# Performance work log

Measured on AMD Instinct MI355X. Metric: run time of the kernel, lower is better.

Reference implementation:

```python
import jax, jax.numpy as jnp
import numpy as np
import math

DIM_K = 64  # head dim used for scaling
NEG = -1000000000.0

def setup_inputs() -> dict:
    key = jax.random.key(0)
    k1, k2, k3, k4 = jax.random.split(key, 4)
    B, H, S, D = 4, 16, 2048, 64
    return {
        "key": jax.random.normal(k1, (B, H, S, D), dtype=jnp.float32),
        "query": jax.random.normal(k2, (B, H, S, D), dtype=jnp.float32),
        "value": jax.random.normal(k3, (B, H, S, D), dtype=jnp.float32),
        "mask": jax.random.randint(k4, (B, S, S), 0, 2, dtype=jnp.int32),
    }

def reference(key, query, value, mask):
    # scores: [B,H,Sq,Sk]
    scores = jnp.einsum('bhqd,bhkd->bhqk', query, key) / math.sqrt(DIM_K)
    scores = jnp.where(mask[:, None, :, :] == 0, NEG, scores)
    attn = jax.nn.softmax(scores, axis=-1)  # dropout is identity in eval mode
    return jnp.einsum('bhqk,bhkd->bhqd', attn, value)
```

## Files before the change

kernel.cpp:

```cpp
#include <hip/hip_runtime.h>
#include <hip/hip_bf16.h>
#include <stdint.h>

#define B_ 4
#define H_ 16
#define S_ 2048
#define D_ 64
#define NKT (S_ / 64)
#define QM 128

typedef __attribute__((ext_vector_type(8))) short bf16x8;
typedef __attribute__((ext_vector_type(4))) float f32x4;
typedef unsigned long long u64;
typedef unsigned int u32;

__device__ inline u32 cvt_pk_bf16(float lo, float hi) {
  u32 r;
  asm("v_cvt_pk_bf16_f32 %0, %1, %2" : "=v"(r) : "v"(lo), "v"(hi));
  return r;
}

__device__ inline int SW(int row, int byteoff) {
  return row * 128 + (byteoff ^ ((row & 7) << 4));
}

__device__ inline void gll16(const void* g, void* l) {
  __builtin_amdgcn_global_load_lds(
      (const __attribute__((address_space(1))) u32*)g,
      (__attribute__((address_space(3))) u32*)(uintptr_t)l, 16, 0, 0);
}

__global__ __launch_bounds__(256)
void prep_k(const float* __restrict__ Kg, char* __restrict__ Ksw) {
  int idx = blockIdx.x * 256 + threadIdx.x;
  int row = idx >> 1, half = idx & 1;
  const float* src = Kg + (size_t)idx * 32;
  float4 v[8];
#pragma unroll
  for (int k = 0; k < 8; ++k) v[k] = *(const float4*)(src + k * 4);
  char* dstrow = Ksw + (size_t)row * 128;
  int xo = (row & 7) << 4;
#pragma unroll
  for (int j = 0; j < 4; ++j) {
    uint4 u;
    u.x = cvt_pk_bf16(v[2 * j].x, v[2 * j].y);
    u.y = cvt_pk_bf16(v[2 * j].z, v[2 * j].w);
    u.z = cvt_pk_bf16(v[2 * j + 1].x, v[2 * j + 1].y);
    u.w = cvt_pk_bf16(v[2 * j + 1].z, v[2 * j + 1].w);
    *(uint4*)(dstrow + (((4 * half + j) * 16) ^ xo)) = u;
  }
}

__global__ __launch_bounds__(256)
void prep_v(const float* __restrict__ Vg, char* __restrict__ Vsw) {
  __shared__ short tile[4096];
  const int vb = blockIdx.x, tid = threadIdx.x;
  char* ct = (char*)tile;
  int c4 = tid & 15, g = tid >> 4;
  const float* src = Vg + (size_t)vb * (64 * D_) + (size_t)(g * 4) * D_ + c4 * 4;
  float4 vv[4];
#pragma unroll
  for (int i = 0; i < 4; ++i) vv[i] = *(const float4*)(src + (size_t)i * D_);
  const float* vf = (const float*)vv;
#pragma unroll
  for (int dd = 0; dd < 4; ++dd) {
    uint2 u;
    u.x = cvt_pk_bf16(vf[0 * 4 + dd], vf[1 * 4 + dd]);
    u.y = cvt_pk_bf16(vf[2 * 4 + dd], vf[3 * 4 + dd]);
    *(uint2*)(ct + SW(c4 * 4 + dd, g * 8)) = u;
  }
  __syncthreads();
  char* dst = Vsw + (size_t)vb * 8192;
#pragma unroll
  for (int j = 0; j < 2; ++j)
    *(float4*)(dst + tid * 16 + j * 4096) = *(const float4*)(ct + tid * 16 + j * 4096);
}

__global__ __launch_bounds__(256)
void prep_m(const int* __restrict__ Mg, u64* __restrict__ Mp) {
  const int tid = threadIdx.x;
  const int lane = tid & 63;
  const int gwave = blockIdx.x * 4 + (tid >> 6);
  for (int c0 = gwave * 4; c0 < (B_ * S_ * S_ / 256); c0 += 4096 * 4) {
    int vals[4][4];
#pragma unroll
    for (int cj = 0; cj < 4; ++cj) {
      const int* src = Mg + (size_t)(c0 + cj) * 256;
#pragma unroll
      for (int j = 0; j < 4; ++j) vals[cj][j] = src[j * 64 + lane];
    }
#pragma unroll
    for (int cj = 0; cj < 4; ++cj) {
      u64 bits[4];
#pragma unroll
      for (int j = 0; j < 4; ++j) bits[j] = __ballot(vals[cj][j] != 0);
      if (lane == 0) {
        ulonglong4 o;
        o.x = bits[0]; o.y = bits[1]; o.z = bits[2]; o.w = bits[3];
        *(ulonglong4*)(Mp + (size_t)(c0 + cj) * 4) = o;
      }
    }
  }
}

__global__ __launch_bounds__(256, 4)
void attn_kernel(const float* __restrict__ Qg,
                 const char* __restrict__ Ksw,
                 const char* __restrict__ Vsw,
                 const u64* __restrict__ Mp,
                 float* __restrict__ Og) {
  __shared__ short sK[2][4096];
  __shared__ short sV[2][4096];

  const int tid  = threadIdx.x;
  const int w    = tid >> 6;
  const int lane = tid & 63;
  const int quad = lane >> 4;
  const int c    = lane & 15;

  const int flat = blockIdx.x + (int)gridDim.x * blockIdx.y;
  const int bh   = (flat & 7) | ((flat >> 7) << 3);
  const int q0   = ((flat >> 3) & 15) * QM;
  const int b    = bh >> 4;

  const size_t base = (size_t)bh * (S_ * D_);
  const char* Kt = Ksw + (size_t)bh * (S_ * 128);
  const char* Vt = Vsw + (size_t)bh * (S_ * 128);
  char* cK0 = (char*)sK;

  const float SC = 0.125f * 1.44269504088896f;
#pragma unroll
  for (int j = 0; j < 8; ++j) {
    int idx = tid + j * 256;
    int row = idx >> 4, c4 = idx & 15;
    float4 v = *(const float4*)(Qg + base + (size_t)(q0 + row) * D_ + c4 * 4);
    uint2 u;
    u.x = cvt_pk_bf16(v.x * SC, v.y * SC);
    u.y = cvt_pk_bf16(v.z * SC, v.w * SC);
    *(uint2*)(cK0 + SW(row, c4 * 8)) = u;
  }
  __syncthreads();
  bf16x8 qa[2][2];
#pragma unroll
  for (int gi = 0; gi < 2; ++gi) {
    qa[gi][0] = *(bf16x8*)(cK0 + SW(32 * w + 16 * gi + c, quad * 16));
    qa[gi][1] = *(bf16x8*)(cK0 + SW(32 * w + 16 * gi + c, 64 + quad * 16));
  }
  __syncthreads();

#pragma unroll
  for (int j = 0; j < 2; ++j) {
    gll16(Kt + tid * 16 + j * 4096, (char*)sK[0] + tid * 16 + j * 4096);
    gll16(Vt + tid * 16 + j * 4096, (char*)sV[0] + tid * 16 + j * 4096);
  }

  int koff[4][2];
#pragma unroll
  for (int n = 0; n < 4; ++n) {
    koff[n][0] = SW(16 * n + c, quad * 16);
    koff[n][1] = SW(16 * n + c, 64 + quad * 16);
  }

  bf16x8 ones;
#pragma unroll
  for (int i = 0; i < 8; ++i) ones[i] = (short)0x3F80;

  f32x4 acco[2][4];
  f32x4 acc_l[2];
#pragma unroll
  for (int gi = 0; gi < 2; ++gi) {
    acc_l[gi] = f32x4{0, 0, 0, 0};
#pragma unroll
    for (int i = 0; i < 4; ++i) acco[gi][i] = f32x4{0, 0, 0, 0};
  }

  const u64* mrowp = Mp + ((size_t)b * S_ + q0 + 32 * w + c) * NKT;

  const char* kbase = (const char*)sK;
  const char* vbase = (const char*)sV;

  for (int kt2 = 0; kt2 < NKT; kt2 += 2) {
#pragma unroll
    for (int p = 0; p < 2; ++p) {
      const int kt = kt2 + p;

      __syncthreads();

      u64 mw[2];
      mw[0] = mrowp[kt];
      mw[1] = mrowp[16 * NKT + kt];

      f32x4 accs[2][4];
      __builtin_amdgcn_s_setprio(1);
#pragma unroll
      for (int n = 0; n < 4; ++n) {
        bf16x8 kb0 = *(bf16x8*)(kbase + koff[n][0] + p * 8192);
        bf16x8 kb1 = *(bf16x8*)(kbase + koff[n][1] + p * 8192);
#pragma unroll
        for (int gi = 0; gi < 2; ++gi) {
          f32x4 z = {0, 0, 0, 0};
          z = __builtin_amdgcn_mfma_f32_16x16x32_bf16(kb0, qa[gi][0], z, 0, 0, 0);
          z = __builtin_amdgcn_mfma_f32_16x16x32_bf16(kb1, qa[gi][1], z, 0, 0, 0);
          accs[gi][n] = z;
        }
      }
      __builtin_amdgcn_s_setprio(0);

      if (kt + 1 < NKT) {
        char* kn = (char*)sK + (p ^ 1) * 8192;
        char* vn = (char*)sV + (p ^ 1) * 8192;
        const char* kg = Kt + (size_t)(kt + 1) * 8192;
        const char* vg = Vt + (size_t)(kt + 1) * 8192;
#pragma unroll
        for (int j = 0; j < 2; ++j) {
          gll16(kg + tid * 16 + j * 4096, kn + tid * 16 + j * 4096);
          gll16(vg + tid * 16 + j * 4096, vn + tid * 16 + j * 4096);
        }
      }

      bf16x8 pa[2][2];
#pragma unroll
      for (int gi = 0; gi < 2; ++gi) {
        u32 mlo = (u32)(mw[gi] >> (4 * quad));
        u32 mhi = (u32)(mw[gi] >> (4 * quad + 32));
        float e[4][4];
#pragma unroll
        for (int n = 0; n < 4; ++n) {
          u32 mword = (n < 2) ? mlo : mhi;
          int sh = 16 * (n & 1);
#pragma unroll
          for (int r = 0; r < 4; ++r) {
            float sm = ((mword >> (sh + r)) & 1u) ? accs[gi][n][r] : -1000.0f;
            e[n][r] = exp2f(sm);
          }
        }

        u32 pk[4][2];
#pragma unroll
        for (int n = 0; n < 4; ++n) {
          pk[n][0] = cvt_pk_bf16(e[n][0], e[n][1]);
          pk[n][1] = cvt_pk_bf16(e[n][2], e[n][3]);
        }

#pragma unroll
        for (int t = 0; t < 2; ++t) {
          union { bf16x8 v; u32 uw[4]; } pu;
#pragma unroll
          for (int h = 0; h < 2; ++h) {
            u32 a  = pk[2 * t][h];
            u32 bq = pk[2 * t + 1][h];
            asm("v_permlane32_swap_b32 %0, %1" : "+v"(a), "+v"(bq));
            asm("v_permlane16_swap_b32 %0, %1" : "+v"(a), "+v"(bq));
            pu.uw[h]     = a;
            pu.uw[2 + h] = bq;
          }
          pa[gi][t] = pu.v;
        }
      }

      __builtin_amdgcn_s_setprio(1);
#pragma unroll
      for (int dn = 0; dn < 4; ++dn) {
        bf16x8 vb0 = *(bf16x8*)(vbase + koff[dn][0] + p * 8192);
        bf16x8 vb1 = *(bf16x8*)(vbase + koff[dn][1] + p * 8192);
#pragma unroll
        for (int gi = 0; gi < 2; ++gi) {
          acco[gi][dn] = __builtin_amdgcn_mfma_f32_16x16x32_bf16(pa[gi][0], vb0, acco[gi][dn], 0, 0, 0);
          acco[gi][dn] = __builtin_amdgcn_mfma_f32_16x16x32_bf16(pa[gi][1], vb1, acco[gi][dn], 0, 0, 0);
        }
      }
#pragma unroll
      for (int gi = 0; gi < 2; ++gi) {
        acc_l[gi] = __builtin_amdgcn_mfma_f32_16x16x32_bf16(pa[gi][0], ones, acc_l[gi], 0, 0, 0);
        acc_l[gi] = __builtin_amdgcn_mfma_f32_16x16x32_bf16(pa[gi][1], ones, acc_l[gi], 0, 0, 0);
      }
      __builtin_amdgcn_s_setprio(0);
    }
  }

#pragma unroll
  for (int gi = 0; gi < 2; ++gi) {
#pragma unroll
    for (int r = 0; r < 4; ++r) {
      float inv = 1.0f / acc_l[gi][r];
      size_t orow = base + (size_t)(q0 + 32 * w + 16 * gi + quad * 4 + r) * D_;
#pragma unroll
      for (int dn = 0; dn < 4; ++dn)
        Og[orow + 16 * dn + c] = acco[gi][dn][r] * inv;
    }
  }
}

extern "C" void kernel_launch(void* const* d_in, const int* in_sizes, int n_in,
                              void* d_out, int out_size, void* d_ws, size_t ws_size,
                              hipStream_t stream) {
  const float* Kg = (const float*)d_in[0];
  const float* Qg = (const float*)d_in[1];
  const float* Vg = (const float*)d_in[2];
  const int*   Mg = (const int*)d_in[3];
  float* Og = (float*)d_out;

  char* ws  = (char*)d_ws;
  u64*  Mp  = (u64*)ws;
  char* Ksw = ws + (size_t)(2u << 20);
  char* Vsw = ws + (size_t)(2u << 20) + (16u << 20);

  prep_k<<<1024, 256, 0, stream>>>(Kg, Ksw);
  prep_v<<<2048, 256, 0, stream>>>(Vg, Vsw);
  prep_m<<<1024, 256, 0, stream>>>(Mg, Mp);
  attn_kernel<<<dim3(S_ / QM, B_ * H_), 256, 0, stream>>>(Qg, Ksw, Vsw, Mp, Og);
}
```

Measured before the change: 305.6 us.

## Split prep and attention into halves and overlap second-half prep with attention

The separate K, V and mask preparation kernels are merged into one device routine that can process either half of the batch-head range. A first kernel preps half 0. A mixed kernel then runs attention on group 0 in 512 blocks while 512 other blocks prep half 1. A final kernel runs attention on group 1. The aim is to hide the memory-bound conversion and mask-packing work behind the compute-bound attention, and to cut the number of launches. The cost is imbalance inside the mixed launch, plus possible contention between attention and prep blocks for memory bandwidth and CU slots.

```diff
diff --git a/kernel.cpp b/kernel.cpp
--- a/kernel.cpp
+++ b/kernel.cpp
@@ -30,96 +30,97 @@
       (__attribute__((address_space(3))) u32*)(uintptr_t)l, 16, 0, 0);
 }
 
-__global__ __launch_bounds__(256)
-void prep_k(const float* __restrict__ Kg, char* __restrict__ Ksw) {
-  int idx = blockIdx.x * 256 + threadIdx.x;
-  int row = idx >> 1, half = idx & 1;
-  const float* src = Kg + (size_t)idx * 32;
-  float4 v[8];
-#pragma unroll
-  for (int k = 0; k < 8; ++k) v[k] = *(const float4*)(src + k * 4);
-  char* dstrow = Ksw + (size_t)row * 128;
-  int xo = (row & 7) << 4;
-#pragma unroll
-  for (int j = 0; j < 4; ++j) {
-    uint4 u;
-    u.x = cvt_pk_bf16(v[2 * j].x, v[2 * j].y);
-    u.y = cvt_pk_bf16(v[2 * j].z, v[2 * j].w);
-    u.z = cvt_pk_bf16(v[2 * j + 1].x, v[2 * j + 1].y);
-    u.w = cvt_pk_bf16(v[2 * j + 1].z, v[2 * j + 1].w);
-    *(uint4*)(dstrow + (((4 * half + j) * 16) ^ xo)) = u;
-  }
-}
-
-__global__ __launch_bounds__(256)
-void prep_v(const float* __restrict__ Vg, char* __restrict__ Vsw) {
-  __shared__ short tile[4096];
-  const int vb = blockIdx.x, tid = threadIdx.x;
-  char* ct = (char*)tile;
-  int c4 = tid & 15, g = tid >> 4;
-  const float* src = Vg + (size_t)vb * (64 * D_) + (size_t)(g * 4) * D_ + c4 * 4;
-  float4 vv[4];
-#pragma unroll
-  for (int i = 0; i < 4; ++i) vv[i] = *(const float4*)(src + (size_t)i * D_);
-  const float* vf = (const float*)vv;
-#pragma unroll
-  for (int dd = 0; dd < 4; ++dd) {
-    uint2 u;
-    u.x = cvt_pk_bf16(vf[0 * 4 + dd], vf[1 * 4 + dd]);
-    u.y = cvt_pk_bf16(vf[2 * 4 + dd], vf[3 * 4 + dd]);
-    *(uint2*)(ct + SW(c4 * 4 + dd, g * 8)) = u;
-  }
-  __syncthreads();
-  char* dst = Vsw + (size_t)vb * 8192;
-#pragma unroll
-  for (int j = 0; j < 2; ++j)
-    *(float4*)(dst + tid * 16 + j * 4096) = *(const float4*)(ct + tid * 16 + j * 4096);
-}
-
-__global__ __launch_bounds__(256)
-void prep_m(const int* __restrict__ Mg, u64* __restrict__ Mp) {
-  const int tid = threadIdx.x;
-  const int lane = tid & 63;
-  const int gwave = blockIdx.x * 4 + (tid >> 6);
-  for (int c0 = gwave * 4; c0 < (B_ * S_ * S_ / 256); c0 += 4096 * 4) {
-    int vals[4][4];
-#pragma unroll
-    for (int cj = 0; cj < 4; ++cj) {
-      const int* src = Mg + (size_t)(c0 + cj) * 256;
-#pragma unroll
-      for (int j = 0; j < 4; ++j) vals[cj][j] = src[j * 64 + lane];
-    }
-#pragma unroll
-    for (int cj = 0; cj < 4; ++cj) {
-      u64 bits[4];
-#pragma unroll
-      for (int j = 0; j < 4; ++j) bits[j] = __ballot(vals[cj][j] != 0);
-      if (lane == 0) {
-        ulonglong4 o;
-        o.x = bits[0]; o.y = bits[1]; o.z = bits[2]; o.w = bits[3];
-        *(ulonglong4*)(Mp + (size_t)(c0 + cj) * 4) = o;
-      }
-    }
-  }
-}
-
-__global__ __launch_bounds__(256, 4)
-void attn_kernel(const float* __restrict__ Qg,
-                 const char* __restrict__ Ksw,
-                 const char* __restrict__ Vsw,
-                 const u64* __restrict__ Mp,
-                 float* __restrict__ Og) {
-  __shared__ short sK[2][4096];
-  __shared__ short sV[2][4096];
-
-  const int tid  = threadIdx.x;
+__device__ inline void dev_prep(int half, int blkL, int tid,
+                                const float* __restrict__ Kg,
+                                const float* __restrict__ Vg,
+                                const int* __restrict__ Mg,
+                                char* __restrict__ Ksw, char* __restrict__ Vsw,
+                                u64* __restrict__ Mp, short* scratch) {
+  {
+    int idxH = half * 131072 + blkL * 256 + tid;
+    int row = idxH >> 1, hh = idxH & 1;
+    const float* src = Kg + (size_t)idxH * 32;
+    float4 v[8];
+#pragma unroll
+    for (int k = 0; k < 8; ++k) v[k] = *(const float4*)(src + k * 4);
+    char* dstrow = Ksw + (size_t)row * 128;
+    int xo = (row & 7) << 4;
+#pragma unroll
+    for (int j = 0; j < 4; ++j) {
+      uint4 u;
+      u.x = cvt_pk_bf16(v[2 * j].x, v[2 * j].y);
+      u.y = cvt_pk_bf16(v[2 * j].z, v[2 * j].w);
+      u.z = cvt_pk_bf16(v[2 * j + 1].x, v[2 * j + 1].y);
+      u.w = cvt_pk_bf16(v[2 * j + 1].z, v[2 * j + 1].w);
+      *(uint4*)(dstrow + (((4 * hh + j) * 16) ^ xo)) = u;
+    }
+  }
+  {
+    char* ct = (char*)scratch;
+    int c4 = tid & 15, g = tid >> 4;
+#pragma unroll
+    for (int it = 0; it < 2; ++it) {
+      int vb = half * 1024 + blkL * 2 + it;
+      const float* src = Vg + (size_t)vb * (64 * D_) + (size_t)(g * 4) * D_ + c4 * 4;
+      float4 vv[4];
+#pragma unroll
+      for (int i = 0; i < 4; ++i) vv[i] = *(const float4*)(src + (size_t)i * D_);
+      const float* vf = (const float*)vv;
+      if (it) __syncthreads();
+#pragma unroll
+      for (int dd = 0; dd < 4; ++dd) {
+        uint2 u;
+        u.x = cvt_pk_bf16(vf[0 * 4 + dd], vf[1 * 4 + dd]);
+        u.y = cvt_pk_bf16(vf[2 * 4 + dd], vf[3 * 4 + dd]);
+        *(uint2*)(ct + SW(c4 * 4 + dd, g * 8)) = u;
+      }
+      __syncthreads();
+      char* dst = Vsw + (size_t)vb * 8192;
+#pragma unroll
+      for (int j = 0; j < 2; ++j)
+        *(float4*)(dst + tid * 16 + j * 4096) = *(const float4*)(ct + tid * 16 + j * 4096);
+    }
+  }
+  {
+    const int lane = tid & 63;
+    const int gw = blkL * 4 + (tid >> 6);
+    const int base = half * 32768;
+    for (int c0 = base + gw * 4; c0 < base + 32768; c0 += 2048 * 4) {
+      int vals[4][4];
+#pragma unroll
+      for (int cj = 0; cj < 4; ++cj) {
+        const int* src = Mg + (size_t)(c0 + cj) * 256;
+#pragma unroll
+        for (int j = 0; j < 4; ++j) vals[cj][j] = src[j * 64 + lane];
+      }
+#pragma unroll
+      for (int cj = 0; cj < 4; ++cj) {
+        u64 bits[4];
+#pragma unroll
+        for (int j = 0; j < 4; ++j) bits[j] = __ballot(vals[cj][j] != 0);
+        if (lane == 0) {
+          ulonglong4 o;
+          o.x = bits[0]; o.y = bits[1]; o.z = bits[2]; o.w = bits[3];
+          *(ulonglong4*)(Mp + (size_t)(c0 + cj) * 4) = o;
+        }
+      }
+    }
+  }
+}
+
+__device__ inline void dev_attn(int group, int flat, int tid,
+                                const float* __restrict__ Qg,
+                                const char* __restrict__ Ksw,
+                                const char* __restrict__ Vsw,
+                                const u64* __restrict__ Mp,
+                                float* __restrict__ Og,
+                                short (*sK)[4096], short (*sV)[4096]) {
   const int w    = tid >> 6;
   const int lane = tid & 63;
   const int quad = lane >> 4;
   const int c    = lane & 15;
 
-  const int flat = blockIdx.x + (int)gridDim.x * blockIdx.y;
-  const int bh   = (flat & 7) | ((flat >> 7) << 3);
+  const int bh   = group * 32 + ((flat & 7) | ((flat >> 7) << 3));
   const int q0   = ((flat >> 3) & 15) * QM;
   const int b    = bh >> 4;
 
@@ -291,6 +292,38 @@
   }
 }
 
+__global__ __launch_bounds__(256, 4)
+void prep_first(const float* __restrict__ Kg, const float* __restrict__ Vg,
+                const int* __restrict__ Mg,
+                char* __restrict__ Ksw, char* __restrict__ Vsw, u64* __restrict__ Mp) {
+  __shared__ short scratch[4096];
+  dev_prep(0, blockIdx.x, threadIdx.x, Kg, Vg, Mg, Ksw, Vsw, Mp, scratch);
+}
+
+__global__ __launch_bounds__(256, 4)
+void attn_mix(const float* __restrict__ Qg,
+              const float* __restrict__ Kg, const float* __restrict__ Vg,
+              const int* __restrict__ Mg,
+              char* __restrict__ Ksw, char* __restrict__ Vsw, u64* __restrict__ Mp,
+              float* __restrict__ Og) {
+  __shared__ short sK[2][4096];
+  __shared__ short sV[2][4096];
+  if (blockIdx.x < 512) {
+    dev_attn(0, blockIdx.x, threadIdx.x, Qg, Ksw, Vsw, Mp, Og, sK, sV);
+  } else {
+    dev_prep(1, blockIdx.x - 512, threadIdx.x, Kg, Vg, Mg, Ksw, Vsw, Mp, (short*)sK);
+  }
+}
+
+__global__ __launch_bounds__(256, 4)
+void attn_last(const float* __restrict__ Qg,
+               const char* __restrict__ Ksw, const char* __restrict__ Vsw,
+               const u64* __restrict__ Mp, float* __restrict__ Og) {
+  __shared__ short sK[2][4096];
+  __shared__ short sV[2][4096];
+  dev_attn(1, blockIdx.x, threadIdx.x, Qg, Ksw, Vsw, Mp, Og, sK, sV);
+}
+
 extern "C" void kernel_launch(void* const* d_in, const int* in_sizes, int n_in,
                               void* d_out, int out_size, void* d_ws, size_t ws_size,
                               hipStream_t stream) {
@@ -305,8 +338,7 @@
   char* Ksw = ws + (size_t)(2u << 20);
   char* Vsw = ws + (size_t)(2u << 20) + (16u << 20);
 
-  prep_k<<<1024, 256, 0, stream>>>(Kg, Ksw);
-  prep_v<<<2048, 256, 0, stream>>>(Vg, Vsw);
-  prep_m<<<1024, 256, 0, stream>>>(Mg, Mp);
-  attn_kernel<<<dim3(S_ / QM, B_ * H_), 256, 0, stream>>>(Qg, Ksw, Vsw, Mp, Og);
-}
+  prep_first<<<512, 256, 0, stream>>>(Kg, Vg, Mg, Ksw, Vsw, Mp);
+  attn_mix<<<1024, 256, 0, stream>>>(Qg, Kg, Vg, Mg, Ksw, Vsw, Mp, Og);
+  attn_last<<<512, 256, 0, stream>>>(Qg, Ksw, Vsw, Mp, Og);
+}
```

New measurement: 366.9 us. +20.0%, slower.
